# Optimization experiments

Measured on AMD Instinct MI355X. Metric: run time of the kernel, lower is better.

The kernel has to match this reference:

```python
import jax, jax.numpy as jnp
import numpy as np


def setup_inputs() -> dict:
    key = jax.random.key(0)
    k1, k2, k3 = jax.random.split(key, 3)
    B, Cin, H, W = 64, 16, 256, 256
    Cout, K = 64, 3
    x = jax.random.normal(k1, (B, Cin, H, W), dtype=jnp.float32)
    # PyTorch Conv2d init scale ~ 1/sqrt(fan_in)
    fan_in = Cin * K * K
    conv_weight = jax.random.normal(k2, (Cout, Cin, K, K), dtype=jnp.float32) / np.sqrt(fan_in)
    conv_bias = jax.random.normal(k3, (Cout,), dtype=jnp.float32) / np.sqrt(fan_in)
    return {"x": x, "conv_weight": conv_weight, "conv_bias": conv_bias}


def reference(x, conv_weight, conv_bias):
    # Conv2d: stride=1, padding=0 (VALID), dilation=1, groups=1
    y = jax.lax.conv_general_dilated(
        x, conv_weight,
        window_strides=(1, 1),
        padding="VALID",
        dimension_numbers=("NCHW", "OIHW", "NCHW"),
    ) + conv_bias[None, :, None, None]          # [B, Cout, 254, 254]
    m = jnp.min(y, axis=1, keepdims=True)        # [B, 1, 254, 254] min over channels
    return jnp.tanh(jnp.tanh(m))                 # double tanh
```

## Files before the change

kernel.cpp:

```cpp
#include <hip/hip_runtime.h>
#include <math.h>

#define CIN    16
#define COUT   64
#define H      256
#define W      256
#define OH     254
#define OW     254
#define NTAP   9
#define RING   6
#define STRIP  32

typedef _Float16 f16x8  __attribute__((ext_vector_type(8)));
typedef float    f32x16 __attribute__((ext_vector_type(16)));

#define XSLOT(w, g) ((((w) << 1) | (g)) ^ (((w) >> 2) & 7))

__global__ void wpack_kernel(const float* __restrict__ w, _Float16* __restrict__ wpk) {
    int idx = blockIdx.x * 256 + threadIdx.x;
    if (idx >= NTAP * 2 * 64 * 8) return;
    int e = idx & 7, l = (idx >> 3) & 63, m = (idx >> 9) & 1, t = idx >> 10;
    int co  = (l & 31) + 32 * m;
    int cin = 8 * (l >> 5) + e;
    wpk[idx] = (_Float16)w[((co * CIN + cin) * 3 + t / 3) * 3 + (t % 3)];
}

__device__ __forceinline__ float tanh_fast(float v) {
    float e = __expf(2.0f * v);
    return 1.0f - 2.0f * __builtin_amdgcn_rcpf(e + 1.0f);
}

__global__ __launch_bounds__(256, 2) void conv_mfma_kernel(
        const float* __restrict__ x, const f16x8* __restrict__ wpk,
        const float* __restrict__ bias, float* __restrict__ out) {
    __shared__ f16x8 xs[RING * 512];

    const int tid = threadIdx.x;
    const int b   = blockIdx.x >> 3;
    const int s   = blockIdx.x & 7;
    const int oh0 = s * STRIP;

    const float* xb = x + (size_t)b * CIN * H * W;
    const int lane = tid & 63;

    f16x8 wreg[NTAP][2];
#pragma unroll
    for (int t = 0; t < NTAP; ++t)
#pragma unroll
        for (int m = 0; m < 2; ++m)
            wreg[t][m] = wpk[(t * 2 + m) * 64 + lane];

    const int wave = tid >> 6;
    const int ph   = wave * 64;
    const int l31  = lane & 31;
    const int g2   = lane >> 5;

    f32x16 cbias[2];
#pragma unroll
    for (int m = 0; m < 2; ++m)
#pragma unroll
        for (int r = 0; r < 16; ++r)
            cbias[m][r] = bias[(r & 3) + 8 * (r >> 2) + 4 * g2 + 32 * m];

    int off[3][2];
#pragma unroll
    for (int kw = 0; kw < 3; ++kw)
#pragma unroll
        for (int n = 0; n < 2; ++n) {
            int w = ph + 32 * n + l31 + kw;
            if (w > 255) w = 255;
            off[kw][n] = XSLOT(w, g2);
        }

#define STAGE_LOAD(rowAbs, v)                                                   \
    {                                                                           \
        int row_ = (rowAbs) > 255 ? 255 : (rowAbs);                             \
        const float* p_ = xb + (size_t)row_ * W + tid;                          \
        _Pragma("unroll")                                                       \
        for (int c = 0; c < CIN; ++c) v[c] = p_[(size_t)c * (H * W)];           \
    }
#define STAGE_WRITE(slot, v)                                                    \
    {                                                                           \
        f16x8 q0, q1;                                                           \
        _Pragma("unroll")                                                       \
        for (int c = 0; c < 8; ++c) { q0[c] = (_Float16)v[c];                   \
                                      q1[c] = (_Float16)v[c + 8]; }             \
        xs[(slot) * 512 + XSLOT(tid, 0)] = q0;                                  \
        xs[(slot) * 512 + XSLOT(tid, 1)] = q1;                                  \
    }

#pragma unroll
    for (int i = 0; i < 4; ++i) {
        float v[CIN];
        STAGE_LOAD(oh0 + i, v)
        STAGE_WRITE(i, v)
    }
    __syncthreads();

    int rs0 = 0, rs1 = 1, rs2 = 2, wsl = 4;

    for (int r = 0; r < STRIP; ++r) {
        float v[CIN];
        STAGE_LOAD(oh0 + r + 4, v)

        const f16x8* x0 = xs + rs0 * 512;
        const f16x8* x1 = xs + rs1 * 512;
        const f16x8* x2 = xs + rs2 * 512;

        f32x16 acc[2][2];
#pragma unroll
        for (int t = 0; t < NTAP; ++t) {
            const int kh = t / 3, kw = t % 3;
            const f16x8* xr = (kh == 0) ? x0 : (kh == 1) ? x1 : x2;
#pragma unroll
            for (int n = 0; n < 2; ++n) {
                f16x8 bf = xr[off[kw][n]];
                if (t == 0) {
                    acc[0][n] = __builtin_amdgcn_mfma_f32_32x32x16_f16(wreg[0][0], bf, cbias[0], 0, 0, 0);
                    acc[1][n] = __builtin_amdgcn_mfma_f32_32x32x16_f16(wreg[0][1], bf, cbias[1], 0, 0, 0);
                } else {
                    acc[0][n] = __builtin_amdgcn_mfma_f32_32x32x16_f16(wreg[t][0], bf, acc[0][n], 0, 0, 0);
                    acc[1][n] = __builtin_amdgcn_mfma_f32_32x32x16_f16(wreg[t][1], bf, acc[1][n], 0, 0, 0);
                }
            }
        }

        const int oh = oh0 + r;
#pragma unroll
        for (int n = 0; n < 2; ++n) {
            float mn = fminf(acc[0][n][0], acc[1][n][0]);
#pragma unroll
            for (int q = 1; q < 16; ++q)
                mn = fminf(mn, fminf(acc[0][n][q], acc[1][n][q]));
            mn = fminf(mn, __shfl_xor(mn, 32));
            float t2 = tanh_fast(tanh_fast(mn));
            int px = ph + 32 * n + l31;
            if (g2 == 0 && px < OW && oh < OH)
                out[((size_t)b * OH + oh) * OW + px] = t2;
        }

        STAGE_WRITE(wsl, v)

        if (r & 1) __syncthreads();

        rs0 = (rs0 == RING - 1) ? 0 : rs0 + 1;
        rs1 = (rs1 == RING - 1) ? 0 : rs1 + 1;
        rs2 = (rs2 == RING - 1) ? 0 : rs2 + 1;
        wsl = (wsl == RING - 1) ? 0 : wsl + 1;
    }
}

extern "C" void kernel_launch(void* const* d_in, const int* in_sizes, int n_in,
                              void* d_out, int out_size, void* d_ws, size_t ws_size,
                              hipStream_t stream) {
    const float* x    = (const float*)d_in[0];
    const float* w    = (const float*)d_in[1];
    const float* bias = (const float*)d_in[2];
    float* out = (float*)d_out;
    _Float16* wpk = (_Float16*)d_ws;

    wpack_kernel<<<36, 256, 0, stream>>>(w, wpk);
    conv_mfma_kernel<<<64 * 8, 256, 0, stream>>>(x, (const f16x8*)wpk, bias, out);
}
```

Measured before the change: 94.37 us.

## Deepen row prefetch to two rows in flight with float2 loads and 8-slot ring

Enlarges the LDS ring to 8 slots so two future input rows are held in registers while the current row is computed, with each loop iteration writing a previously loaded row to LDS and then issuing the next load. Global loads change from 16 scalar floats per thread to 8 float2 loads, splitting the channels between the two thread halves. Slot indices become compile-time masks through a 2x manual unroll, and one barrier covers every two rows. The aim is to hide global load latency behind the MFMA work, at the cost of more registers for the extra prefetch buffer and more LDS.

Result: no change. 92.73 us (-1.7%).

```diff
diff --git a/kernel.cpp b/kernel.cpp
--- a/kernel.cpp
+++ b/kernel.cpp
@@ -8,7 +8,7 @@
 #define OH     254
 #define OW     254
 #define NTAP   9
-#define RING   6
+#define RING   8
 #define STRIP  32
 
 typedef _Float16 f16x8  __attribute__((ext_vector_type(8)));
@@ -72,81 +72,86 @@
             off[kw][n] = XSLOT(w, g2);
         }
 
+    const int gld = tid >> 7;
+    const int w2  = (tid & 127) * 2;
+
 #define STAGE_LOAD(rowAbs, v)                                                   \
     {                                                                           \
         int row_ = (rowAbs) > 255 ? 255 : (rowAbs);                             \
-        const float* p_ = xb + (size_t)row_ * W + tid;                          \
+        const float* p_ = xb + (size_t)row_ * W + w2;                           \
         _Pragma("unroll")                                                       \
-        for (int c = 0; c < CIN; ++c) v[c] = p_[(size_t)c * (H * W)];           \
+        for (int c = 0; c < 8; ++c)                                             \
+            v[c] = *(const float2*)(p_ + (size_t)(8 * gld + c) * (H * W));      \
     }
 #define STAGE_WRITE(slot, v)                                                    \
     {                                                                           \
         f16x8 q0, q1;                                                           \
         _Pragma("unroll")                                                       \
-        for (int c = 0; c < 8; ++c) { q0[c] = (_Float16)v[c];                   \
-                                      q1[c] = (_Float16)v[c + 8]; }             \
-        xs[(slot) * 512 + XSLOT(tid, 0)] = q0;                                  \
-        xs[(slot) * 512 + XSLOT(tid, 1)] = q1;                                  \
+        for (int c = 0; c < 8; ++c) { q0[c] = (_Float16)v[c].x;                 \
+                                      q1[c] = (_Float16)v[c].y; }               \
+        xs[(slot) * 512 + XSLOT(w2,     gld)] = q0;                             \
+        xs[(slot) * 512 + XSLOT(w2 + 1, gld)] = q1;                             \
     }
 
-#pragma unroll
-    for (int i = 0; i < 4; ++i) {
-        float v[CIN];
-        STAGE_LOAD(oh0 + i, v)
-        STAGE_WRITE(i, v)
+    {
+        float2 v0[8], v1[8], v2[8], v3[8];
+        STAGE_LOAD(oh0 + 0, v0)
+        STAGE_LOAD(oh0 + 1, v1)
+        STAGE_LOAD(oh0 + 2, v2)
+        STAGE_LOAD(oh0 + 3, v3)
+        STAGE_WRITE(0, v0)
+        STAGE_WRITE(1, v1)
+        STAGE_WRITE(2, v2)
+        STAGE_WRITE(3, v3)
     }
+    float2 vvA[8], vvB[8];
+    STAGE_LOAD(oh0 + 4, vvA)
+    STAGE_LOAD(oh0 + 5, vvB)
     __syncthreads();
 
-    int rs0 = 0, rs1 = 1, rs2 = 2, wsl = 4;
+#define ITER(r, vv)                                                             \
+    {                                                                           \
+        if ((r) + 4 <= STRIP + 1) STAGE_WRITE(((r) + 4) & 7, vv)                \
+        if ((r) + 6 <= STRIP + 1) STAGE_LOAD(oh0 + (r) + 6, vv)                 \
+        const f16x8* x0 = xs + (((r)    ) & 7) * 512;                           \
+        const f16x8* x1 = xs + (((r) + 1) & 7) * 512;                           \
+        const f16x8* x2 = xs + (((r) + 2) & 7) * 512;                           \
+        f32x16 acc[2][2];                                                       \
+        _Pragma("unroll")                                                       \
+        for (int t = 0; t < NTAP; ++t) {                                        \
+            const int kh = t / 3, kw = t % 3;                                   \
+            const f16x8* xr = (kh == 0) ? x0 : (kh == 1) ? x1 : x2;             \
+            _Pragma("unroll")                                                   \
+            for (int n = 0; n < 2; ++n) {                                       \
+                f16x8 bf = xr[off[kw][n]];                                      \
+                if (t == 0) {                                                   \
+                    acc[0][n] = __builtin_amdgcn_mfma_f32_32x32x16_f16(wreg[0][0], bf, cbias[0], 0, 0, 0); \
+                    acc[1][n] = __builtin_amdgcn_mfma_f32_32x32x16_f16(wreg[0][1], bf, cbias[1], 0, 0, 0); \
+                } else {                                                        \
+                    acc[0][n] = __builtin_amdgcn_mfma_f32_32x32x16_f16(wreg[t][0], bf, acc[0][n], 0, 0, 0); \
+                    acc[1][n] = __builtin_amdgcn_mfma_f32_32x32x16_f16(wreg[t][1], bf, acc[1][n], 0, 0, 0); \
+                }                                                               \
+            }                                                                   \
+        }                                                                       \
+        const int oh = oh0 + (r);                                               \
+        _Pragma("unroll")                                                       \
+        for (int n = 0; n < 2; ++n) {                                           \
+            float mn = fminf(acc[0][n][0], acc[1][n][0]);                       \
+            _Pragma("unroll")                                                   \
+            for (int q = 1; q < 16; ++q)                                        \
+                mn = fminf(mn, fminf(acc[0][n][q], acc[1][n][q]));              \
+            mn = fminf(mn, __shfl_xor(mn, 32));                                 \
+            float t2 = tanh_fast(tanh_fast(mn));                                \
+            int px = ph + 32 * n + l31;                                         \
+            if (g2 == 0 && px < OW && oh < OH)                                  \
+                out[((size_t)b * OH + oh) * OW + px] = t2;                      \
+        }                                                                       \
+    }
 
-    for (int r = 0; r < STRIP; ++r) {
-        float v[CIN];
-        STAGE_LOAD(oh0 + r + 4, v)
-
-        const f16x8* x0 = xs + rs0 * 512;
-        const f16x8* x1 = xs + rs1 * 512;
-        const f16x8* x2 = xs + rs2 * 512;
-
-        f32x16 acc[2][2];
-#pragma unroll
-        for (int t = 0; t < NTAP; ++t) {
-            const int kh = t / 3, kw = t % 3;
-            const f16x8* xr = (kh == 0) ? x0 : (kh == 1) ? x1 : x2;
-#pragma unroll
-            for (int n = 0; n < 2; ++n) {
-                f16x8 bf = xr[off[kw][n]];
-                if (t == 0) {
-                    acc[0][n] = __builtin_amdgcn_mfma_f32_32x32x16_f16(wreg[0][0], bf, cbias[0], 0, 0, 0);
-                    acc[1][n] = __builtin_amdgcn_mfma_f32_32x32x16_f16(wreg[0][1], bf, cbias[1], 0, 0, 0);
-                } else {
-                    acc[0][n] = __builtin_amdgcn_mfma_f32_32x32x16_f16(wreg[t][0], bf, acc[0][n], 0, 0, 0);
-                    acc[1][n] = __builtin_amdgcn_mfma_f32_32x32x16_f16(wreg[t][1], bf, acc[1][n], 0, 0, 0);
-                }
-            }
-        }
-
-        const int oh = oh0 + r;
-#pragma unroll
-        for (int n = 0; n < 2; ++n) {
-            float mn = fminf(acc[0][n][0], acc[1][n][0]);
-#pragma unroll
-            for (int q = 1; q < 16; ++q)
-                mn = fminf(mn, fminf(acc[0][n][q], acc[1][n][q]));
-            mn = fminf(mn, __shfl_xor(mn, 32));
-            float t2 = tanh_fast(tanh_fast(mn));
-            int px = ph + 32 * n + l31;
-            if (g2 == 0 && px < OW && oh < OH)
-                out[((size_t)b * OH + oh) * OW + px] = t2;
-        }
-
-        STAGE_WRITE(wsl, v)
-
-        if (r & 1) __syncthreads();
-
-        rs0 = (rs0 == RING - 1) ? 0 : rs0 + 1;
-        rs1 = (rs1 == RING - 1) ? 0 : rs1 + 1;
-        rs2 = (rs2 == RING - 1) ? 0 : rs2 + 1;
-        wsl = (wsl == RING - 1) ? 0 : wsl + 1;
+    for (int rr = 0; rr < STRIP; rr += 2) {
+        ITER(rr,     vvA)
+        ITER(rr + 1, vvB)
+        __syncthreads();
     }
 }
 
```

## Give each wave a private LDS ring with halo columns and drop block barriers

Applied to the files above, without the earlier changes.

Each wave now stages only its own 64-pixel column slice, plus a two-pixel halo, into a private 4-slot LDS ring. This removes every __syncthreads from the row loop. Global loads become float2 per lane across 8 channels, with half the lanes fetching the halo values. The next row is written between the kh=0/1 and kh=2 MFMA groups and loaded during the epilogue, and the channel-min reduction uses a shallower min3 tree. The cost is redundant halo loads at wave boundaries, a more complex LDS indexing scheme, and reliance on intra-wave ordering for LDS correctness.

Result: no change. 92.84 us (-1.6%).

```diff
diff --git a/kernel.cpp b/kernel.cpp
--- a/kernel.cpp
+++ b/kernel.cpp
@@ -8,13 +8,12 @@
 #define OH     254
 #define OW     254
 #define NTAP   9
-#define RING   6
 #define STRIP  32
 
 typedef _Float16 f16x8  __attribute__((ext_vector_type(8)));
 typedef float    f32x16 __attribute__((ext_vector_type(16)));
 
-#define XSLOT(w, g) ((((w) << 1) | (g)) ^ (((w) >> 2) & 7))
+#define XS(px, g) ((((px) << 1) | (g)) ^ (((px) >> 2) & 7))
 
 __global__ void wpack_kernel(const float* __restrict__ w, _Float16* __restrict__ wpk) {
     int idx = blockIdx.x * 256 + threadIdx.x;
@@ -29,19 +28,24 @@
     float e = __expf(2.0f * v);
     return 1.0f - 2.0f * __builtin_amdgcn_rcpf(e + 1.0f);
 }
+__device__ __forceinline__ float min3f(float a, float b, float c) {
+    return fminf(fminf(a, b), c);
+}
 
 __global__ __launch_bounds__(256, 2) void conv_mfma_kernel(
         const float* __restrict__ x, const f16x8* __restrict__ wpk,
         const float* __restrict__ bias, float* __restrict__ out) {
-    __shared__ f16x8 xs[RING * 512];
+    __shared__ f16x8 xs[4 * 4 * 136];
 
-    const int tid = threadIdx.x;
-    const int b   = blockIdx.x >> 3;
-    const int s   = blockIdx.x & 7;
-    const int oh0 = s * STRIP;
+    const int tid  = threadIdx.x;
+    const int lane = tid & 63;
+    const int wave = tid >> 6;
+    const int b    = blockIdx.x >> 3;
+    const int s    = blockIdx.x & 7;
+    const int oh0  = s * STRIP;
+    const int P    = wave * 64;
 
     const float* xb = x + (size_t)b * CIN * H * W;
-    const int lane = tid & 63;
 
     f16x8 wreg[NTAP][2];
 #pragma unroll
@@ -50,10 +54,28 @@
         for (int m = 0; m < 2; ++m)
             wreg[t][m] = wpk[(t * 2 + m) * 64 + lane];
 
-    const int wave = tid >> 6;
-    const int ph   = wave * 64;
-    const int l31  = lane & 31;
-    const int g2   = lane >> 5;
+    const int l31 = lane & 31;
+    const int g2  = lane >> 5;
+    const int px2 = 2 * l31;
+
+    f16x8*    xw  = xs + wave * 544;
+    _Float16* xwh = (_Float16*)xw;
+
+    const int wr0 = XS(px2, g2);
+    const int wr1 = XS(px2 + 1, g2);
+    const bool hsel = (lane < 32);
+    int hpx = P + 64 + (lane & 1); if (hpx > 255) hpx = 255;
+    const int hcin = (lane & 31) >> 1;
+    const int hoff = 1056 + (lane & 1) * 16 + hcin;
+
+    int off[3][2];
+#pragma unroll
+    for (int kw = 0; kw < 3; ++kw)
+#pragma unroll
+        for (int n = 0; n < 2; ++n) {
+            int px = 32 * n + l31 + kw;
+            off[kw][n] = (px < 64) ? XS(px, g2) : (132 + (px - 64) * 2 + g2);
+        }
 
     f32x16 cbias[2];
 #pragma unroll
@@ -62,56 +84,46 @@
         for (int r = 0; r < 16; ++r)
             cbias[m][r] = bias[(r & 3) + 8 * (r >> 2) + 4 * g2 + 32 * m];
 
-    int off[3][2];
-#pragma unroll
-    for (int kw = 0; kw < 3; ++kw)
-#pragma unroll
-        for (int n = 0; n < 2; ++n) {
-            int w = ph + 32 * n + l31 + kw;
-            if (w > 255) w = 255;
-            off[kw][n] = XSLOT(w, g2);
-        }
+    float2 vv[8];
+    float  vh;
 
-#define STAGE_LOAD(rowAbs, v)                                                   \
+#define SLOAD(rowAbs)                                                           \
     {                                                                           \
-        int row_ = (rowAbs) > 255 ? 255 : (rowAbs);                             \
-        const float* p_ = xb + (size_t)row_ * W + tid;                          \
+        int r_ = (rowAbs) > 255 ? 255 : (rowAbs);                               \
+        const float* p_ = xb + (size_t)r_ * W;                                  \
         _Pragma("unroll")                                                       \
-        for (int c = 0; c < CIN; ++c) v[c] = p_[(size_t)c * (H * W)];           \
+        for (int c = 0; c < 8; ++c)                                             \
+            vv[c] = *(const float2*)(p_ + (size_t)(8 * g2 + c) * (H * W) + P + px2); \
+        if (hsel) vh = p_[(size_t)hcin * (H * W) + hpx];                        \
     }
-#define STAGE_WRITE(slot, v)                                                    \
+
+#define SWRITE(slot)                                                            \
     {                                                                           \
         f16x8 q0, q1;                                                           \
         _Pragma("unroll")                                                       \
-        for (int c = 0; c < 8; ++c) { q0[c] = (_Float16)v[c];                   \
-                                      q1[c] = (_Float16)v[c + 8]; }             \
-        xs[(slot) * 512 + XSLOT(tid, 0)] = q0;                                  \
-        xs[(slot) * 512 + XSLOT(tid, 1)] = q1;                                  \
+        for (int c = 0; c < 8; ++c) { q0[c] = (_Float16)vv[c].x;                \
+                                      q1[c] = (_Float16)vv[c].y; }              \
+        xw[(slot) * 136 + wr0] = q0;                                            \
+        xw[(slot) * 136 + wr1] = q1;                                            \
+        if (hsel) xwh[(slot) * 1088 + hoff] = (_Float16)vh;                     \
     }
 
-#pragma unroll
-    for (int i = 0; i < 4; ++i) {
-        float v[CIN];
-        STAGE_LOAD(oh0 + i, v)
-        STAGE_WRITE(i, v)
-    }
-    __syncthreads();
+    SLOAD(oh0 + 0) SWRITE(0)
+    SLOAD(oh0 + 1) SWRITE(1)
+    SLOAD(oh0 + 2) SWRITE(2)
+    SLOAD(oh0 + 3)
 
-    int rs0 = 0, rs1 = 1, rs2 = 2, wsl = 4;
-
+#pragma unroll 1
     for (int r = 0; r < STRIP; ++r) {
-        float v[CIN];
-        STAGE_LOAD(oh0 + r + 4, v)
-
-        const f16x8* x0 = xs + rs0 * 512;
-        const f16x8* x1 = xs + rs1 * 512;
-        const f16x8* x2 = xs + rs2 * 512;
+        const f16x8* xr0 = xw + ((r    ) & 3) * 136;
+        const f16x8* xr1 = xw + ((r + 1) & 3) * 136;
+        const f16x8* xr2 = xw + ((r + 2) & 3) * 136;
 
         f32x16 acc[2][2];
 #pragma unroll
-        for (int t = 0; t < NTAP; ++t) {
-            const int kh = t / 3, kw = t % 3;
-            const f16x8* xr = (kh == 0) ? x0 : (kh == 1) ? x1 : x2;
+        for (int t = 0; t < 6; ++t) {
+            const int kw = t % 3;
+            const f16x8* xr = (t < 3) ? xr0 : xr1;
 #pragma unroll
             for (int n = 0; n < 2; ++n) {
                 f16x8 bf = xr[off[kw][n]];
@@ -125,28 +137,40 @@
             }
         }
 
+        SWRITE((r + 3) & 3)
+
+#pragma unroll
+        for (int t = 6; t < 9; ++t) {
+            const int kw = t % 3;
+#pragma unroll
+            for (int n = 0; n < 2; ++n) {
+                f16x8 bf = xr2[off[kw][n]];
+                acc[0][n] = __builtin_amdgcn_mfma_f32_32x32x16_f16(wreg[t][0], bf, acc[0][n], 0, 0, 0);
+                acc[1][n] = __builtin_amdgcn_mfma_f32_32x32x16_f16(wreg[t][1], bf, acc[1][n], 0, 0, 0);
+            }
+        }
+
+        SLOAD(oh0 + r + 4)
+
         const int oh = oh0 + r;
 #pragma unroll
         for (int n = 0; n < 2; ++n) {
-            float mn = fminf(acc[0][n][0], acc[1][n][0]);
+            float tq[16];
 #pragma unroll
-            for (int q = 1; q < 16; ++q)
-                mn = fminf(mn, fminf(acc[0][n][q], acc[1][n][q]));
+            for (int q = 0; q < 16; ++q)
+                tq[q] = fminf(acc[0][n][q], acc[1][n][q]);
+            float a  = min3f(tq[0],  tq[1],  tq[2]);
+            float b2 = min3f(tq[3],  tq[4],  tq[5]);
+            float c  = min3f(tq[6],  tq[7],  tq[8]);
+            float d  = min3f(tq[9],  tq[10], tq[11]);
+            float e  = min3f(tq[12], tq[13], tq[14]);
+            float mn = fminf(min3f(a, b2, c), min3f(d, e, tq[15]));
             mn = fminf(mn, __shfl_xor(mn, 32));
             float t2 = tanh_fast(tanh_fast(mn));
-            int px = ph + 32 * n + l31;
+            int px = P + 32 * n + l31;
             if (g2 == 0 && px < OW && oh < OH)
                 out[((size_t)b * OH + oh) * OW + px] = t2;
         }
-
-        STAGE_WRITE(wsl, v)
-
-        if (r & 1) __syncthreads();
-
-        rs0 = (rs0 == RING - 1) ? 0 : rs0 + 1;
-        rs1 = (rs1 == RING - 1) ? 0 : rs1 + 1;
-        rs2 = (rs2 == RING - 1) ? 0 : rs2 + 1;
-        wsl = (wsl == RING - 1) ? 0 : wsl + 1;
     }
 }
 
```

## Split rows into 12 exact strips, move half weights to LDS, raise occupancy

Applied to the files above, without the earlier changes.

Partitions the 254 output rows into 12 strips of 21 or 22 rows per batch, so no wasted rows are computed, and launches 768 blocks with a swizzled block-to-work mapping. The second half of the weights moves from registers into shared memory, bias is reloaded per row instead of held in registers, and the ring shrinks to 4 slots. Together these cut register and LDS use so launch bounds can target 3 blocks per CU. Input staging now uses float2 loads split over channel halves. In exchange there are more LDS reads per tap, a barrier on every row, and a shallower prefetch.

Result: slower. 121.9 us (+29.2%).

```diff
diff --git a/kernel.cpp b/kernel.cpp
--- a/kernel.cpp
+++ b/kernel.cpp
@@ -8,13 +8,12 @@
 #define OH     254
 #define OW     254
 #define NTAP   9
-#define RING   6
-#define STRIP  32
+#define RING   4
 
 typedef _Float16 f16x8  __attribute__((ext_vector_type(8)));
 typedef float    f32x16 __attribute__((ext_vector_type(16)));
 
-#define XSLOT(w, g) ((((w) << 1) | (g)) ^ (((w) >> 2) & 7))
+#define XS(px, g) ((((px) << 1) | (g)) ^ (((px) >> 2) & 7))
 
 __global__ void wpack_kernel(const float* __restrict__ w, _Float16* __restrict__ wpk) {
     int idx = blockIdx.x * 256 + threadIdx.x;
@@ -29,124 +28,128 @@
     float e = __expf(2.0f * v);
     return 1.0f - 2.0f * __builtin_amdgcn_rcpf(e + 1.0f);
 }
+__device__ __forceinline__ float min3f(float a, float b, float c) {
+    return fminf(fminf(a, b), c);
+}
 
-__global__ __launch_bounds__(256, 2) void conv_mfma_kernel(
+__global__ __launch_bounds__(256, 3) void conv_mfma_kernel(
         const float* __restrict__ x, const f16x8* __restrict__ wpk,
         const float* __restrict__ bias, float* __restrict__ out) {
     __shared__ f16x8 xs[RING * 512];
+    __shared__ f16x8 wl[NTAP * 64];
 
-    const int tid = threadIdx.x;
-    const int b   = blockIdx.x >> 3;
-    const int s   = blockIdx.x & 7;
-    const int oh0 = s * STRIP;
+    const int tid  = threadIdx.x;
+    const int lane = tid & 63;
+
+    int bid = blockIdx.x;
+    int nb  = (bid & 7) * 96 + (bid >> 3);
+    int b   = nb / 12;
+    int s   = nb - 12 * b;
+    const int h  = (s < 2) ? 22 : 21;
+    const int r0 = (s < 2) ? 22 * s : 44 + 21 * (s - 2);
 
     const float* xb = x + (size_t)b * CIN * H * W;
-    const int lane = tid & 63;
 
-    f16x8 wreg[NTAP][2];
+    f16x8 wreg[NTAP];
 #pragma unroll
-    for (int t = 0; t < NTAP; ++t)
+    for (int t = 0; t < NTAP; ++t) wreg[t] = wpk[(t * 2) * 64 + lane];
+    for (int i = tid; i < NTAP * 64; i += 256)
+        wl[i] = wpk[((i >> 6) * 2 + 1) * 64 + (i & 63)];
+
+    const int g   = tid >> 7;
+    const int w2  = (tid & 127) * 2;
+    const int wv  = tid >> 6;
+    const int l31 = lane & 31;
+    const int g2  = lane >> 5;
+    const int P   = wv * 64;
+
+    float2 vv[8];
+
+#define SLOAD(rowAbs)                                                           \
+    {                                                                           \
+        int r_ = (rowAbs) > 255 ? 255 : (rowAbs);                               \
+        const float* p_ = xb + (size_t)r_ * W + w2;                             \
+        _Pragma("unroll")                                                       \
+        for (int c = 0; c < 8; ++c)                                             \
+            vv[c] = *(const float2*)(p_ + (size_t)(8 * g + c) * (H * W));       \
+    }
+#define SWRITE(slot)                                                            \
+    {                                                                           \
+        f16x8 q0, q1;                                                           \
+        _Pragma("unroll")                                                       \
+        for (int c = 0; c < 8; ++c) { q0[c] = (_Float16)vv[c].x;                \
+                                      q1[c] = (_Float16)vv[c].y; }              \
+        xs[(slot) * 512 + XS(w2,     g)] = q0;                                  \
+        xs[(slot) * 512 + XS(w2 + 1, g)] = q1;                                  \
+    }
+
 #pragma unroll
-        for (int m = 0; m < 2; ++m)
-            wreg[t][m] = wpk[(t * 2 + m) * 64 + lane];
-
-    const int wave = tid >> 6;
-    const int ph   = wave * 64;
-    const int l31  = lane & 31;
-    const int g2   = lane >> 5;
-
-    f32x16 cbias[2];
-#pragma unroll
-    for (int m = 0; m < 2; ++m)
-#pragma unroll
-        for (int r = 0; r < 16; ++r)
-            cbias[m][r] = bias[(r & 3) + 8 * (r >> 2) + 4 * g2 + 32 * m];
+    for (int i = 0; i < 3; ++i) { SLOAD(r0 + i) SWRITE(i) }
+    __syncthreads();
 
     int off[3][2];
 #pragma unroll
     for (int kw = 0; kw < 3; ++kw)
 #pragma unroll
         for (int n = 0; n < 2; ++n) {
-            int w = ph + 32 * n + l31 + kw;
-            if (w > 255) w = 255;
-            off[kw][n] = XSLOT(w, g2);
+            int px = P + 32 * n + l31 + kw;
+            if (px > 255) px = 255;
+            off[kw][n] = XS(px, g2);
         }
 
-#define STAGE_LOAD(rowAbs, v)                                                   \
-    {                                                                           \
-        int row_ = (rowAbs) > 255 ? 255 : (rowAbs);                             \
-        const float* p_ = xb + (size_t)row_ * W + tid;                          \
-        _Pragma("unroll")                                                       \
-        for (int c = 0; c < CIN; ++c) v[c] = p_[(size_t)c * (H * W)];           \
-    }
-#define STAGE_WRITE(slot, v)                                                    \
-    {                                                                           \
-        f16x8 q0, q1;                                                           \
-        _Pragma("unroll")                                                       \
-        for (int c = 0; c < 8; ++c) { q0[c] = (_Float16)v[c];                   \
-                                      q1[c] = (_Float16)v[c + 8]; }             \
-        xs[(slot) * 512 + XSLOT(tid, 0)] = q0;                                  \
-        xs[(slot) * 512 + XSLOT(tid, 1)] = q1;                                  \
-    }
+#pragma unroll 1
+    for (int r = 0; r < h; ++r) {
+        const bool doStage = (r + 3 <= h + 1);
+        if (doStage) SLOAD(r0 + r + 3)
 
+        f32x16 cb0, cb1;
 #pragma unroll
-    for (int i = 0; i < 4; ++i) {
-        float v[CIN];
-        STAGE_LOAD(oh0 + i, v)
-        STAGE_WRITE(i, v)
-    }
-    __syncthreads();
+        for (int q = 0; q < 16; ++q) {
+            const int i0 = (q & 3) + 8 * (q >> 2);
+            cb0[q] = g2 ? bias[i0 + 4]  : bias[i0];
+            cb1[q] = g2 ? bias[i0 + 36] : bias[i0 + 32];
+        }
 
-    int rs0 = 0, rs1 = 1, rs2 = 2, wsl = 4;
-
-    for (int r = 0; r < STRIP; ++r) {
-        float v[CIN];
-        STAGE_LOAD(oh0 + r + 4, v)
-
-        const f16x8* x0 = xs + rs0 * 512;
-        const f16x8* x1 = xs + rs1 * 512;
-        const f16x8* x2 = xs + rs2 * 512;
+        const f16x8* xr0 = xs + ((r    ) & 3) * 512;
+        const f16x8* xr1 = xs + ((r + 1) & 3) * 512;
+        const f16x8* xr2 = xs + ((r + 2) & 3) * 512;
 
         f32x16 acc[2][2];
 #pragma unroll
         for (int t = 0; t < NTAP; ++t) {
             const int kh = t / 3, kw = t % 3;
-            const f16x8* xr = (kh == 0) ? x0 : (kh == 1) ? x1 : x2;
+            const f16x8* xr = (kh == 0) ? xr0 : (kh == 1) ? xr1 : xr2;
+            f16x8 a1 = wl[t * 64 + lane];
 #pragma unroll
             for (int n = 0; n < 2; ++n) {
                 f16x8 bf = xr[off[kw][n]];
                 if (t == 0) {
-                    acc[0][n] = __builtin_amdgcn_mfma_f32_32x32x16_f16(wreg[0][0], bf, cbias[0], 0, 0, 0);
-                    acc[1][n] = __builtin_amdgcn_mfma_f32_32x32x16_f16(wreg[0][1], bf, cbias[1], 0, 0, 0);
+                    acc[0][n] = __builtin_amdgcn_mfma_f32_32x32x16_f16(wreg[0], bf, cb0, 0, 0, 0);
+                    acc[1][n] = __builtin_amdgcn_mfma_f32_32x32x16_f16(a1,      bf, cb1, 0, 0, 0);
                 } else {
-                    acc[0][n] = __builtin_amdgcn_mfma_f32_32x32x16_f16(wreg[t][0], bf, acc[0][n], 0, 0, 0);
-                    acc[1][n] = __builtin_amdgcn_mfma_f32_32x32x16_f16(wreg[t][1], bf, acc[1][n], 0, 0, 0);
+                    acc[0][n] = __builtin_amdgcn_mfma_f32_32x32x16_f16(wreg[t], bf, acc[0][n], 0, 0, 0);
+                    acc[1][n] = __builtin_amdgcn_mfma_f32_32x32x16_f16(a1,      bf, acc[1][n], 0, 0, 0);
                 }
             }
         }
 
-        const int oh = oh0 + r;
+        const int oh = r0 + r;
 #pragma unroll
         for (int n = 0; n < 2; ++n) {
             float mn = fminf(acc[0][n][0], acc[1][n][0]);
 #pragma unroll
             for (int q = 1; q < 16; ++q)
-                mn = fminf(mn, fminf(acc[0][n][q], acc[1][n][q]));
+                mn = min3f(acc[0][n][q], acc[1][n][q], mn);
             mn = fminf(mn, __shfl_xor(mn, 32));
             float t2 = tanh_fast(tanh_fast(mn));
-            int px = ph + 32 * n + l31;
-            if (g2 == 0 && px < OW && oh < OH)
+            int px = P + 32 * n + l31;
+            if (g2 == 0 && px < OW)
                 out[((size_t)b * OH + oh) * OW + px] = t2;
         }
 
-        STAGE_WRITE(wsl, v)
+        if (doStage) SWRITE((r + 3) & 3)
 
-        if (r & 1) __syncthreads();
-
-        rs0 = (rs0 == RING - 1) ? 0 : rs0 + 1;
-        rs1 = (rs1 == RING - 1) ? 0 : rs1 + 1;
-        rs2 = (rs2 == RING - 1) ? 0 : rs2 + 1;
-        wsl = (wsl == RING - 1) ? 0 : wsl + 1;
+        __syncthreads();
     }
 }
 
@@ -160,5 +163,5 @@
     _Float16* wpk = (_Float16*)d_ws;
 
     wpack_kernel<<<36, 256, 0, stream>>>(w, wpk);
-    conv_mfma_kernel<<<64 * 8, 256, 0, stream>>>(x, (const f16x8*)wpk, bias, out);
+    conv_mfma_kernel<<<64 * 12, 256, 0, stream>>>(x, (const f16x8*)wpk, bias, out);
 }
```
